# Kernel optimization log

Measured on AMD Instinct MI355X. Metric: run time of the kernel, lower is better.

## Reference

```python
import jax, jax.numpy as jnp
import numpy as np

NUM_HEADS = 8
WINDOW = 3
LOCAL_LEN = WINDOW * WINDOW
SR_RATIO = 8


def _normalize(v, eps=1e-12):
    n = jnp.linalg.norm(v, axis=-1, keepdims=True)
    return v / jnp.maximum(n, eps)


def _layernorm(v, g, b, eps=1e-5):
    m = v.mean(-1, keepdims=True)
    var = ((v - m) ** 2).mean(-1, keepdims=True)
    return (v - m) / jnp.sqrt(var + eps) * g + b


def _unfold3(x, H, W):
    # x: [B, C, H, W] -> [B, C, 9, H*W]  (kernel 3, pad 1, stride 1; torch nn.Unfold layout)
    B, C = x.shape[0], x.shape[1]
    xp = jnp.pad(x, ((0, 0), (0, 0), (1, 1), (1, 1)))
    patches = jnp.stack([xp[:, :, di:di + H, dj:dj + W]
                         for di in range(WINDOW) for dj in range(WINDOW)], axis=2)
    return patches.reshape(B, C, LOCAL_LEN, H * W)


def _forward(x, relative_coords_table, seq_length_scale, q_w, q_b, kv_w, kv_b,
             temperature, query_embedding, sr_w, sr_b, norm_g, norm_b,
             cpb_fc1_w, cpb_fc1_b, cpb_fc2_w, cpb_fc2_b,
             rel_bias_local, learnable_tokens, learnable_bias,
             proj_w, proj_b, relative_pos_index, padding_mask, H, W):
    B, N, C = x.shape
    hd = C // NUM_HEADS
    pool_H, pool_W = H // SR_RATIO, W // SR_RATIO
    pool_len = pool_H * pool_W

    # ---- queries ----
    q = (x @ q_w.T + q_b).reshape(B, N, NUM_HEADS, hd).transpose(0, 2, 1, 3)  # [B,h,N,d]
    q_norm = _normalize(q)
    q_scaled = (q_norm + query_embedding) * jax.nn.softplus(temperature) * seq_length_scale

    # ---- local k/v via unfold ----
    kv = x @ kv_w.T + kv_b  # [B,N,2C]
    k_loc = _normalize(kv[..., :C].reshape(B, N, NUM_HEADS, hd)).reshape(B, N, C)
    kv_img = jnp.concatenate([k_loc, kv[..., C:]], -1).transpose(0, 2, 1).reshape(B, 2 * C, H, W)
    kv_unf = _unfold3(kv_img, H, W).reshape(B, 2 * NUM_HEADS, hd, LOCAL_LEN, N)
    kv_unf = kv_unf.transpose(0, 1, 4, 2, 3)  # [B,2h,N,d,9]
    k_local, v_local = kv_unf[:, :NUM_HEADS], kv_unf[:, NUM_HEADS:]

    attn_local = jnp.einsum('bhnd,bhndl->bhnl', q_scaled, k_local) + rel_bias_local[:, None, :]
    attn_local = jnp.where(padding_mask, -jnp.inf, attn_local)

    # ---- pooled global k/v ----
    x_img = x.transpose(0, 2, 1).reshape(B, C, H, W)
    x_sr = jax.nn.gelu(jnp.einsum('oc,bchw->bohw', sr_w, x_img) + sr_b[None, :, None, None],
                       approximate=False)
    x_pool = x_sr.reshape(B, C, pool_H, SR_RATIO, pool_W, SR_RATIO).mean((3, 5))
    x_pool = x_pool.reshape(B, C, pool_len).transpose(0, 2, 1)
    x_pool = _layernorm(x_pool, norm_g, norm_b)
    kv_p = (x_pool @ kv_w.T + kv_b).reshape(B, pool_len, 2 * NUM_HEADS, hd).transpose(0, 2, 1, 3)
    k_pool, v_pool = kv_p[:, :NUM_HEADS], kv_p[:, NUM_HEADS:]

    # ---- continuous relative position bias (extrapolation path) ----
    cpb = jax.nn.relu(relative_coords_table @ cpb_fc1_w.T + cpb_fc1_b) @ cpb_fc2_w.T + cpb_fc2_b  # [T,h]
    pool_bias = cpb[relative_pos_index].reshape(N, pool_len, NUM_HEADS).transpose(2, 0, 1)  # [h,N,P]

    attn_pool = jnp.einsum('bhnd,bhpd->bhnp', q_scaled, _normalize(k_pool)) + pool_bias

    attn = jax.nn.softmax(jnp.concatenate([attn_local, attn_pool], -1), axis=-1)
    a_loc, a_pool = attn[..., :LOCAL_LEN], attn[..., LOCAL_LEN:]

    lt = jnp.einsum('bhnd,hdl->bhnl', q_norm, learnable_tokens) + learnable_bias + a_loc
    x_local = jnp.einsum('bhnl,bhndl->bhnd', lt, v_local)
    x_p = jnp.einsum('bhnp,bhpd->bhnd', a_pool, v_pool)
    out = (x_local + x_p).transpose(0, 2, 1, 3).reshape(B, N, C)
    return out @ proj_w.T + proj_b


def setup_inputs() -> dict:
    key = jax.random.key(0)
    B, H, W, C = 4, 64, 64, 256
    N = H * W
    hd = C // NUM_HEADS
    pool_H, pool_W = H // SR_RATIO, W // SR_RATIO
    pool_len = pool_H * pool_W

    # padding mask + per-query valid window length (get_seqlen_and_mask)
    ii, jj = np.meshgrid(np.arange(H), np.arange(W), indexing='ij')
    cols = []
    for di in range(WINDOW):
        for dj in range(WINDOW):
            ni, nj = ii + di - 1, jj + dj - 1
            cols.append(((ni < 0) | (ni >= H) | (nj < 0) | (nj >= W)).reshape(-1))
    padding_mask = np.stack(cols, -1)  # [N, 9], True = outside image
    local_len = (~padding_mask).sum(-1, keepdims=True).astype(np.float32)
    seq_length_scale = np.log(local_len + pool_len)  # [N, 1]

    # get_relative_position_cpb((H,W), (pool_H,pool_W))
    axis_q = np.arange(H, dtype=np.float64)
    axis_k = axis_q.reshape(pool_H, SR_RATIO).mean(-1)
    kh, kw = np.meshgrid(axis_k, axis_k, indexing='ij')
    qh, qw = np.meshgrid(axis_q, axis_q, indexing='ij')
    rel_h = (qh.ravel()[:, None] - kh.ravel()[None, :]) / (H - 1) * 8
    rel_w = (qw.ravel()[:, None] - kw.ravel()[None, :]) / (W - 1) * 8
    rel = np.stack([rel_h, rel_w], -1).reshape(-1, 2)
    table, idx = np.unique(rel, axis=0, return_inverse=True)
    table = np.sign(table) * np.log2(np.abs(table) + 1.0) / np.log2(8.0)

    ks = jax.random.split(key, 12)

    def nrm(k, shape, std=0.02):
        return jax.random.normal(k, shape, jnp.float32) * std

    return {
        'x': jax.random.normal(ks[0], (B, N, C), jnp.float32),
        'relative_coords_table': jnp.asarray(table, jnp.float32),
        'seq_length_scale': jnp.asarray(seq_length_scale, jnp.float32),
        'q_w': nrm(ks[1], (C, C)), 'q_b': jnp.zeros((C,), jnp.float32),
        'kv_w': nrm(ks[2], (2 * C, C)), 'kv_b': jnp.zeros((2 * C,), jnp.float32),
        'temperature': jnp.full((NUM_HEADS, 1, 1), float(np.log(np.expm1(1.0 / 0.24))), jnp.float32),
        'query_embedding': nrm(ks[3], (NUM_HEADS, 1, hd)),
        'sr_w': nrm(ks[4], (C, C)), 'sr_b': jnp.zeros((C,), jnp.float32),
        'norm_g': jnp.ones((C,), jnp.float32), 'norm_b': jnp.zeros((C,), jnp.float32),
        'cpb_fc1_w': nrm(ks[5], (512, 2), 0.1), 'cpb_fc1_b': jnp.zeros((512,), jnp.float32),
        'cpb_fc2_w': nrm(ks[6], (NUM_HEADS, 512)), 'cpb_fc2_b': jnp.zeros((NUM_HEADS,), jnp.float32),
        'rel_bias_local': nrm(ks[7], (NUM_HEADS, LOCAL_LEN), 0.0004),
        'learnable_tokens': nrm(ks[8], (NUM_HEADS, hd, LOCAL_LEN)),
        'learnable_bias': jnp.zeros((NUM_HEADS, 1, LOCAL_LEN), jnp.float32),
        'proj_w': nrm(ks[9], (C, C)), 'proj_b': jnp.zeros((C,), jnp.float32),
        'relative_pos_index': jnp.asarray(idx, jnp.int32),
        'padding_mask': jnp.asarray(padding_mask),
        'H': H, 'W': W,
    }


def reference(x, relative_coords_table, seq_length_scale, q_w, q_b, kv_w, kv_b,
              temperature, query_embedding, sr_w, sr_b, norm_g, norm_b,
              cpb_fc1_w, cpb_fc1_b, cpb_fc2_w, cpb_fc2_b,
              rel_bias_local, learnable_tokens, learnable_bias,
              proj_w, proj_b, relative_pos_index, padding_mask, H, W):
    return _forward(x, relative_coords_table, seq_length_scale, q_w, q_b, kv_w, kv_b,
                    temperature, query_embedding, sr_w, sr_b, norm_g, norm_b,
                    cpb_fc1_w, cpb_fc1_b, cpb_fc2_w, cpb_fc2_b,
                    rel_bias_local, learnable_tokens, learnable_bias,
                    proj_w, proj_b, relative_pos_index, padding_mask, H, W)
```

## Files before the change

### kernel.cpp

```cpp
#include <hip/hip_runtime.h>
#include <math.h>


typedef unsigned short ushort_t;
typedef __attribute__((ext_vector_type(8))) _Float16 half8;
typedef __attribute__((ext_vector_type(2))) _Float16 half2_t;
typedef __attribute__((ext_vector_type(4))) float f32x4;

static __device__ __forceinline__ ushort_t f2h(float f) {
    _Float16 h = (_Float16)f;
    return *(ushort_t*)&h;
}

static __device__ __forceinline__ float fdot2f(half2_t a, half2_t b, float c) {
#if __has_builtin(__builtin_amdgcn_fdot2)
    return __builtin_amdgcn_fdot2(a, b, c, false);
#else
    return (float)a[0] * (float)b[0] + (float)a[1] * (float)b[1] + c;
#endif
}

#define GLOAD16(g, l)                                                        \
    __builtin_amdgcn_global_load_lds(                                        \
        (const __attribute__((address_space(1))) unsigned int*)(g),          \
        (__attribute__((address_space(3))) unsigned int*)(l), 16, 0, 0)

template <int TM>
__global__ __launch_bounds__(256) void mfma_hgemm(
    const ushort_t* __restrict__ Ag, const ushort_t* __restrict__ Bg,
    const float* __restrict__ bias, float* __restrict__ out0,
    ushort_t* __restrict__ kvh, float* __restrict__ out2, int mode)
{
    const int K = 256;
    const int IM = TM / 32;
    __shared__ ushort_t Ah[TM * 32];
    __shared__ ushort_t Bh[64 * 32];

    const int t = threadIdx.x;
    const int w = t >> 6;
    const int lane = t & 63;
    const int bm = blockIdx.y * TM;
    const int bn = blockIdx.x * 64;
    const int wm = (w >> 1) * (TM / 2);
    const int wn = (w & 1) * 32;

    f32x4 acc[IM][2];
#pragma unroll
    for (int i = 0; i < IM; ++i)
#pragma unroll
        for (int j = 0; j < 2; ++j) acc[i][j] = f32x4{0.f, 0.f, 0.f, 0.f};

    const int lrow = t >> 2;
    const int lk8  = (t & 3) * 8;

    for (int k0 = 0; k0 < K; k0 += 32) {
#pragma unroll
        for (int r = 0; r < TM / 64; ++r) {
            GLOAD16(Ag + (size_t)(bm + r * 64 + lrow) * K + k0 + lk8,
                    &Ah[(unsigned)(r * 64 + (w * 16)) * 32]);
        }
        GLOAD16(Bg + (size_t)(bn + lrow) * K + k0 + lk8,
                &Bh[(unsigned)(w * 16) * 32]);
        __syncthreads();

        const int fr = lane & 15;
        const int fq = (lane >> 4) * 8;
        half8 af[IM], bf[2];
#pragma unroll
        for (int i = 0; i < IM; ++i)
            af[i] = *(const half8*)&Ah[(wm + i * 16 + fr) * 32 + fq];
#pragma unroll
        for (int j = 0; j < 2; ++j)
            bf[j] = *(const half8*)&Bh[(wn + j * 16 + fr) * 32 + fq];
#pragma unroll
        for (int i = 0; i < IM; ++i)
#pragma unroll
            for (int j = 0; j < 2; ++j)
                acc[i][j] = __builtin_amdgcn_mfma_f32_16x16x32_f16(af[i], bf[j], acc[i][j], 0, 0, 0);
        __syncthreads();
    }

    const int fr = lane & 15;
    const int q4 = (lane >> 4) * 4;
#pragma unroll
    for (int i = 0; i < IM; ++i) {
#pragma unroll
        for (int j = 0; j < 2; ++j) {
            const int col = bn + wn + j * 16 + fr;
            const float bv = bias[col];
#pragma unroll
            for (int r = 0; r < 4; ++r) {
                const int row = bm + wm + i * 16 + q4 + r;
                float v = acc[i][j][r] + bv;
                if (mode == 0) {
                    if (col < 256)      out0[(size_t)row * 256 + col] = v;
                    else if (col < 768) kvh[(size_t)row * 512 + (col - 256)] = f2h(v);
                    else {
                        v = 0.5f * v * (1.0f + erff(v * 0.70710678118654752f));
                        out2[(size_t)row * 256 + (col - 768)] = v;
                    }
                } else {
                    out0[(size_t)row * 256 + col] = v;
                }
            }
        }
    }
}

__global__ __launch_bounds__(256) void cast_half(
    const float4* __restrict__ x, ushort4* __restrict__ o, int n4)
{
    int i = blockIdx.x * 256 + threadIdx.x;
    if (i >= n4) return;
    float4 v = x[i];
    ushort4 h;
    h.x = f2h(v.x); h.y = f2h(v.y); h.z = f2h(v.z); h.w = f2h(v.w);
    o[i] = h;
}

__global__ __launch_bounds__(256) void pack_weights2(
    const float* __restrict__ qw, const float* __restrict__ kvw,
    const float* __restrict__ srw, const float* __restrict__ pw,
    const float* __restrict__ qb, const float* __restrict__ kvb,
    const float* __restrict__ srb,
    ushort_t* __restrict__ Wall, ushort_t* __restrict__ Pw,
    float* __restrict__ ball)
{
    int idx = blockIdx.x * 256 + threadIdx.x;
    if (idx < 262144) {
        int nn = idx >> 8, k = idx & 255;
        float a;
        if (nn < 256)      a = qw[nn * 256 + k];
        else if (nn < 768) a = kvw[(nn - 256) * 256 + k];
        else               a = srw[(nn - 768) * 256 + k];
        Wall[idx] = f2h(a);
    }
    if (idx < 65536) Pw[idx] = f2h(pw[idx]);
    if (idx < 1024) {
        float bv;
        if (idx < 256)      bv = qb[idx];
        else if (idx < 768) bv = kvb[idx - 256];
        else                bv = srb[idx - 768];
        ball[idx] = bv;
    }
}

__global__ __launch_bounds__(256) void bias_expand_t(
    const int* __restrict__ rpi, const float* __restrict__ cpbT,
    float* __restrict__ pbias)
{
    int idx = blockIdx.x * 256 + threadIdx.x;
    int h = idx >> 18;
    int np = idx & 262143;
    pbias[idx] = cpbT[(size_t)rpi[np] * 8 + h];
}

#define BM 64
#define BN 64
#define BKK 16
__global__ __launch_bounds__(256) void gemm_bias_act(
    const float* __restrict__ A, const float* __restrict__ Wt,
    const float* __restrict__ bias, float* __restrict__ Cmat,
    int M, int N, int K, int act)
{
    __shared__ float As[BKK][BM + 4];
    __shared__ float Bs[BKK][BN + 4];
    const int tid = threadIdx.x;
    const int bm = blockIdx.y * BM;
    const int bn = blockIdx.x * BN;
    const int tr = (tid >> 4) << 2;
    const int tc = (tid & 15) << 2;
    const int lr = tid >> 2;
    const int lc = (tid & 3) << 2;
    float acc[4][4] = {{0.f}};

    for (int k0 = 0; k0 < K; k0 += BKK) {
        float4 av = *(const float4*)(A  + (size_t)(bm + lr) * K + k0 + lc);
        float4 wv = *(const float4*)(Wt + (size_t)(bn + lr) * K + k0 + lc);
        As[lc + 0][lr] = av.x; As[lc + 1][lr] = av.y;
        As[lc + 2][lr] = av.z; As[lc + 3][lr] = av.w;
        Bs[lc + 0][lr] = wv.x; Bs[lc + 1][lr] = wv.y;
        Bs[lc + 2][lr] = wv.z; Bs[lc + 3][lr] = wv.w;
        __syncthreads();
#pragma unroll
        for (int kk = 0; kk < BKK; ++kk) {
            float4 a  = *(const float4*)&As[kk][tr];
            float4 bq = *(const float4*)&Bs[kk][tc];
            float av4[4] = {a.x, a.y, a.z, a.w};
            float bv4[4] = {bq.x, bq.y, bq.z, bq.w};
#pragma unroll
            for (int ii = 0; ii < 4; ++ii)
#pragma unroll
                for (int jj = 0; jj < 4; ++jj)
                    acc[ii][jj] = fmaf(av4[ii], bv4[jj], acc[ii][jj]);
        }
        __syncthreads();
    }
#pragma unroll
    for (int ii = 0; ii < 4; ++ii) {
        int m = bm + tr + ii;
#pragma unroll
        for (int jj = 0; jj < 4; ++jj) {
            int nn = bn + tc + jj;
            float v = acc[ii][jj] + bias[nn];
            if (act == 1) v = 0.5f * v * (1.0f + erff(v * 0.70710678118654752f));
            Cmat[(size_t)m * N + nn] = v;
        }
    }
}

__global__ __launch_bounds__(256) void headnorm(float* __restrict__ buf, int rowStride)
{
    size_t row = blockIdx.x;
    int tid = threadIdx.x;
    float* p = buf + row * (size_t)rowStride + tid;
    float v = *p;
    float ss = v * v;
#pragma unroll
    for (int off = 16; off; off >>= 1) ss += __shfl_xor(ss, off, 32);
    *p = v / fmaxf(sqrtf(ss), 1e-12f);
}

__global__ __launch_bounds__(256) void headnorm_h(ushort_t* __restrict__ buf)
{
    size_t row = blockIdx.x;
    int tid = threadIdx.x;
    ushort_t* p = buf + row * 512 + tid;
    float v = (float)(*(const _Float16*)p);
    float ss = v * v;
#pragma unroll
    for (int off = 16; off; off >>= 1) ss += __shfl_xor(ss, off, 32);
    *p = f2h(v / fmaxf(sqrtf(ss), 1e-12f));
}

__global__ __launch_bounds__(256) void pool_ln(
    const float* __restrict__ xsr, const float* __restrict__ g,
    const float* __restrict__ be, float* __restrict__ xpool, int Hh, int Ww)
{
    const int C = 256;
    const int Nn = Hh * Ww;
    int b = blockIdx.x >> 6;
    int pidx = blockIdx.x & 63;
    int ph = pidx >> 3, pw = pidx & 7;
    int tid = threadIdx.x;
    float s = 0.f;
    for (int si = 0; si < 8; ++si) {
        int i = ph * 8 + si;
        const float* rowp = xsr + ((size_t)b * Nn + (size_t)i * Ww + pw * 8) * C + tid;
#pragma unroll
        for (int sj = 0; sj < 8; ++sj) s += rowp[(size_t)sj * C];
    }
    s *= (1.f / 64.f);
    __shared__ float red[256];
    red[tid] = s; __syncthreads();
    for (int st = 128; st; st >>= 1) { if (tid < st) red[tid] += red[tid + st]; __syncthreads(); }
    float mean = red[0] * (1.f / 256.f);
    __syncthreads();
    float dv = s - mean;
    red[tid] = dv * dv; __syncthreads();
    for (int st = 128; st; st >>= 1) { if (tid < st) red[tid] += red[tid + st]; __syncthreads(); }
    float var = red[0] * (1.f / 256.f);
    xpool[(size_t)blockIdx.x * C + tid] = dv * rsqrtf(var + 1e-5f) * g[tid] + be[tid];
}

__global__ __launch_bounds__(256) void cpb_mlp_v2(
    const float* __restrict__ table, const float* __restrict__ w1,
    const float* __restrict__ b1, const float* __restrict__ w2,
    const float* __restrict__ b2, float* __restrict__ outc, int T)
{
    const int wv = threadIdx.x >> 6;
    const int lane = threadIdx.x & 63;
    const int row = blockIdx.x * 4 + wv;
    if (row >= T) return;
    const float t0 = table[(size_t)row * 2];
    const float t1 = table[(size_t)row * 2 + 1];
    const int base = lane * 8;

    const float4* w1p = (const float4*)(w1 + (size_t)base * 2);
    float4 wa = w1p[0], wb = w1p[1], wc = w1p[2], wd = w1p[3];
    float4 ba = *(const float4*)(b1 + base);
    float4 bb = *(const float4*)(b1 + base + 4);
    float h[8];
    h[0] = fmaxf(fmaf(t1, wa.y, fmaf(t0, wa.x, ba.x)), 0.f);
    h[1] = fmaxf(fmaf(t1, wa.w, fmaf(t0, wa.z, ba.y)), 0.f);
    h[2] = fmaxf(fmaf(t1, wb.y, fmaf(t0, wb.x, ba.z)), 0.f);
    h[3] = fmaxf(fmaf(t1, wb.w, fmaf(t0, wb.z, ba.w)), 0.f);
    h[4] = fmaxf(fmaf(t1, wc.y, fmaf(t0, wc.x, bb.x)), 0.f);
    h[5] = fmaxf(fmaf(t1, wc.w, fmaf(t0, wc.z, bb.y)), 0.f);
    h[6] = fmaxf(fmaf(t1, wd.y, fmaf(t0, wd.x, bb.z)), 0.f);
    h[7] = fmaxf(fmaf(t1, wd.w, fmaf(t0, wd.z, bb.w)), 0.f);

#pragma unroll
    for (int hh = 0; hh < 8; ++hh) {
        const float4* w2p = (const float4*)(w2 + (size_t)hh * 512 + base);
        float4 p0 = w2p[0], p1 = w2p[1];
        float s = h[0]*p0.x + h[1]*p0.y + h[2]*p0.z + h[3]*p0.w
                + h[4]*p1.x + h[5]*p1.y + h[6]*p1.z + h[7]*p1.w;
#pragma unroll
        for (int off = 1; off <= 32; off <<= 1) s += __shfl_xor(s, off);
        if (lane == 0) outc[(size_t)row * 8 + hh] = s + b2[hh];
    }
}

__global__ __launch_bounds__(256) void attn_v7(
    const float* __restrict__ qraw,
    const ushort_t* __restrict__ kvh,
    const float* __restrict__ kvp,
    const float* __restrict__ pbias,
    const float* __restrict__ sls, const float* __restrict__ temp,
    const float* __restrict__ qe, const float* __restrict__ rbl,
    const float* __restrict__ ltok, const float* __restrict__ lbias,
    ushort_t* __restrict__ attno_hf)
{
    const int h = blockIdx.y, b = blockIdx.z;
    const int t = threadIdx.x;

    __shared__ half8 kp_s[64][4];
    __shared__ half8 vp_s[64][4];
    __shared__ float lts[9][32];
    __shared__ float rbl_s[9], lb_s[9], qe_s[32];

    {
        const int p = t >> 2;
        const int g4 = t & 3;
        const float* g = kvp + ((size_t)(b * 64 + p)) * 512 + h * 32 + g4 * 8;
        float4 ka = *(const float4*)(g + 0);
        float4 kb = *(const float4*)(g + 4);
        float4 va = *(const float4*)(g + 256);
        float4 vb = *(const float4*)(g + 260);
        half8 kh, vh;
        kh[0]=(_Float16)ka.x; kh[1]=(_Float16)ka.y; kh[2]=(_Float16)ka.z; kh[3]=(_Float16)ka.w;
        kh[4]=(_Float16)kb.x; kh[5]=(_Float16)kb.y; kh[6]=(_Float16)kb.z; kh[7]=(_Float16)kb.w;
        vh[0]=(_Float16)va.x; vh[1]=(_Float16)va.y; vh[2]=(_Float16)va.z; vh[3]=(_Float16)va.w;
        vh[4]=(_Float16)vb.x; vh[5]=(_Float16)vb.y; vh[6]=(_Float16)vb.z; vh[7]=(_Float16)vb.w;
        kp_s[p][g4] = kh;
        vp_s[p][g4] = vh;
        for (int u = t; u < 288; u += 256) lts[u % 9][u / 9] = ltok[h * 288 + u];
        if (t < 9)  { rbl_s[t] = rbl[h * 9 + t]; lb_s[t] = lbias[h * 9 + t]; }
        if (t >= 64 && t < 96) qe_s[t - 64] = qe[h * 32 + (t - 64)];
    }
    __syncthreads();

    const int w = t >> 6;
    const int lane = t & 63;
    const int qi = lane >> 2;
    const int g4 = lane & 3;
    const int co = g4 * 8;
    const int i = blockIdx.x;
    const int j = w * 16 + qi;
    const int n = i * 64 + j;
    const size_t gq = (size_t)b * 4096 + n;

    const float tm = temp[h];
    const float sp = (tm > 20.f) ? tm : log1pf(expf(tm));

    float qv[8];
    {
        float ss = 0.f;
        const float4* qp = (const float4*)(qraw + gq * 256 + h * 32 + co);
#pragma unroll
        for (int c4 = 0; c4 < 2; ++c4) {
            float4 v = qp[c4];
            qv[4*c4+0] = v.x; qv[4*c4+1] = v.y; qv[4*c4+2] = v.z; qv[4*c4+3] = v.w;
            ss += v.x*v.x + v.y*v.y + v.z*v.z + v.w*v.w;
        }
        ss += __shfl_xor(ss, 1);
        ss += __shfl_xor(ss, 2);
        const float invn = 1.0f / fmaxf(sqrtf(ss), 1e-12f);
#pragma unroll
        for (int d = 0; d < 8; ++d) qv[d] *= invn;
    }

    float lt[9];
#pragma unroll
    for (int l = 0; l < 9; ++l) {
        float dl = 0.f;
        const float4* lw = (const float4*)&lts[l][co];
#pragma unroll
        for (int c4 = 0; c4 < 2; ++c4) {
            float4 w4 = lw[c4];
            dl += qv[4*c4+0]*w4.x + qv[4*c4+1]*w4.y + qv[4*c4+2]*w4.z + qv[4*c4+3]*w4.w;
        }
        dl += __shfl_xor(dl, 1);
        dl += __shfl_xor(dl, 2);
        lt[l] = dl + lb_s[l];
    }

    const float scal = sp * sls[n];
    half2_t qh[4];
#pragma unroll
    for (int c = 0; c < 4; ++c) {
        float a = (qv[2*c+0] + qe_s[co + 2*c+0]) * scal;
        float bq = (qv[2*c+1] + qe_s[co + 2*c+1]) * scal;
        qh[c] = half2_t{(_Float16)a, (_Float16)bq};
    }

    float sl[9];
#pragma unroll
    for (int l = 0; l < 9; ++l) {
        const int di = l / 3 - 1, dj = l % 3 - 1;
        const int ii = i + di;
        const int jn = j + dj;
        const bool ok = (ii >= 0) && (ii < 64) && (jn >= 0) && (jn < 64);
        const int ic = max(min(ii, 63), 0);
        const int jc = max(min(jn, 63), 0);
        const half8 k8 = *(const half8*)(kvh + ((size_t)(b * 4096 + ic * 64 + jc)) * 512 + h * 32 + co);
        float dk = 0.f;
        dk = fdot2f(qh[0], __builtin_shufflevector(k8, k8, 0, 1), dk);
        dk = fdot2f(qh[1], __builtin_shufflevector(k8, k8, 2, 3), dk);
        dk = fdot2f(qh[2], __builtin_shufflevector(k8, k8, 4, 5), dk);
        dk = fdot2f(qh[3], __builtin_shufflevector(k8, k8, 6, 7), dk);
        dk += __shfl_xor(dk, 1);
        dk += __shfl_xor(dk, 2);
        sl[l] = ok ? (dk + rbl_s[l]) : -INFINITY;
    }

    float m = sl[0];
#pragma unroll
    for (int l = 1; l < 9; ++l) m = fmaxf(m, sl[l]);

    half2_t oh[4];
#pragma unroll
    for (int c = 0; c < 4; ++c) oh[c] = half2_t{(_Float16)0.f, (_Float16)0.f};
    float Z = 0.f;
    const float* plane = pbias + ((size_t)h << 18) + (size_t)n * 64;

    for (int cch = 0; cch < 8; ++cch) {
        float s8[8];
        float4 pb0 = *(const float4*)(plane + cch * 8);
        float4 pb1 = *(const float4*)(plane + cch * 8 + 4);
        const float pbv[8] = {pb0.x, pb0.y, pb0.z, pb0.w, pb1.x, pb1.y, pb1.z, pb1.w};
#pragma unroll
        for (int k = 0; k < 8; ++k) {
            const int p = cch * 8 + k;
            const half8 k8 = kp_s[p][g4];
            float acc = 0.f;
            acc = fdot2f(qh[0], __builtin_shufflevector(k8, k8, 0, 1), acc);
            acc = fdot2f(qh[1], __builtin_shufflevector(k8, k8, 2, 3), acc);
            acc = fdot2f(qh[2], __builtin_shufflevector(k8, k8, 4, 5), acc);
            acc = fdot2f(qh[3], __builtin_shufflevector(k8, k8, 6, 7), acc);
            acc += __shfl_xor(acc, 1);
            acc += __shfl_xor(acc, 2);
            s8[k] = acc + pbv[k];
        }
        float cmax = s8[0];
#pragma unroll
        for (int k = 1; k < 8; ++k) cmax = fmaxf(cmax, s8[k]);
        const float m_new = fmaxf(m, cmax);
        const float factor = __expf(m - m_new);
        Z *= factor;
        const _Float16 fh = (_Float16)factor;
        const half2_t f2 = half2_t{fh, fh};
#pragma unroll
        for (int c = 0; c < 4; ++c) oh[c] *= f2;
        m = m_new;
#pragma unroll
        for (int k = 0; k < 8; ++k) {
            const float a = __expf(s8[k] - m);
            Z += a;
            const _Float16 ah = (_Float16)a;
            const half2_t a2 = half2_t{ah, ah};
            const half8 v8 = vp_s[cch * 8 + k][g4];
            oh[0] = a2 * __builtin_shufflevector(v8, v8, 0, 1) + oh[0];
            oh[1] = a2 * __builtin_shufflevector(v8, v8, 2, 3) + oh[1];
            oh[2] = a2 * __builtin_shufflevector(v8, v8, 4, 5) + oh[2];
            oh[3] = a2 * __builtin_shufflevector(v8, v8, 6, 7) + oh[3];
        }
    }

#pragma unroll
    for (int l = 0; l < 9; ++l) { sl[l] = __expf(sl[l] - m); Z += sl[l]; }

#pragma unroll
    for (int l = 0; l < 9; ++l) {
        const int di = l / 3 - 1, dj = l % 3 - 1;
        const int ii = i + di;
        const int jn = j + dj;
        const bool ok = (ii >= 0) && (ii < 64) && (jn >= 0) && (jn < 64);
        const int ic = max(min(ii, 63), 0);
        const int jc = max(min(jn, 63), 0);
        const float coef = ok ? (sl[l] + lt[l] * Z) : 0.f;
        const half8 v8 = *(const half8*)(kvh + ((size_t)(b * 4096 + ic * 64 + jc)) * 512 + 256 + h * 32 + co);
        const _Float16 ch = (_Float16)coef;
        const half2_t c2 = half2_t{ch, ch};
        oh[0] = c2 * __builtin_shufflevector(v8, v8, 0, 1) + oh[0];
        oh[1] = c2 * __builtin_shufflevector(v8, v8, 2, 3) + oh[1];
        oh[2] = c2 * __builtin_shufflevector(v8, v8, 4, 5) + oh[2];
        oh[3] = c2 * __builtin_shufflevector(v8, v8, 6, 7) + oh[3];
    }

    const float invZ = 1.0f / Z;
    ushort4* outp = (ushort4*)(attno_hf + gq * 256 + h * 32 + co);
#pragma unroll
    for (int c4 = 0; c4 < 2; ++c4) {
        ushort4 u;
        u.x = f2h((float)oh[2*c4+0][0] * invZ);
        u.y = f2h((float)oh[2*c4+0][1] * invZ);
        u.z = f2h((float)oh[2*c4+1][0] * invZ);
        u.w = f2h((float)oh[2*c4+1][1] * invZ);
        outp[c4] = u;
    }
}

extern "C" void kernel_launch(void* const* d_in, const int* in_sizes, int n_in,
                              void* d_out, int out_size, void* d_ws, size_t ws_size,
                              hipStream_t stream)
{
    const float* x    = (const float*)d_in[0];
    const float* tbl  = (const float*)d_in[1];
    const float* sls  = (const float*)d_in[2];
    const float* q_w  = (const float*)d_in[3];
    const float* q_b  = (const float*)d_in[4];
    const float* kv_w = (const float*)d_in[5];
    const float* kv_b = (const float*)d_in[6];
    const float* temp = (const float*)d_in[7];
    const float* qe   = (const float*)d_in[8];
    const float* sr_w = (const float*)d_in[9];
    const float* sr_b = (const float*)d_in[10];
    const float* ng   = (const float*)d_in[11];
    const float* nb   = (const float*)d_in[12];
    const float* f1w  = (const float*)d_in[13];
    const float* f1b  = (const float*)d_in[14];
    const float* f2w  = (const float*)d_in[15];
    const float* f2b  = (const float*)d_in[16];
    const float* rbl  = (const float*)d_in[17];
    const float* ltok = (const float*)d_in[18];
    const float* lbias= (const float*)d_in[19];
    const float* pw   = (const float*)d_in[20];
    const float* pb   = (const float*)d_in[21];
    const int*   rpi  = (const int*)d_in[22];

    const int C = 256, Hh = 64, Ww = 64, Nn = Hh * Ww;
    const int B = in_sizes[0] / (Nn * C);
    const int T = in_sizes[1] / 2;
    const int M = B * Nn;

    float* ws = (float*)d_ws;
    size_t o = 0;
    float* qbuf  = ws + o; o += (size_t)M * C;
    ushort_t* kvh = (ushort_t*)(ws + o); o += (size_t)M * C;
    float* xsr   = ws + o; o += (size_t)M * C;
    float* xpool = ws + o; o += (size_t)B * 64 * C;
    float* kvp   = ws + o; o += (size_t)B * 64 * 2 * C;
    float* cpbB  = ws + o; o += (size_t)T * 8;
    float* pbias = ws + o; o += (size_t)8 * Nn * 64;
    ushort_t* xh   = (ushort_t*)(ws + o); o += (size_t)M * C / 2;
    ushort_t* Wall = (ushort_t*)(ws + o); o += 1024 * 256 / 2;
    ushort_t* Pwh  = (ushort_t*)(ws + o); o += 256 * 256 / 2;
    float* ball = ws + o; o += 1024;
    ushort_t* attno_hf = xh;

    dim3 blk(256);
    const int n4x = M * C / 4;

    cast_half<<<(n4x + 255) / 256, blk, 0, stream>>>((const float4*)x, (ushort4*)xh, n4x);
    pack_weights2<<<1024, blk, 0, stream>>>(q_w, kv_w, sr_w, pw, q_b, kv_b, sr_b,
                                            Wall, Pwh, ball);
    mfma_hgemm<128><<<dim3(16, M / 128), blk, 0, stream>>>(
        xh, Wall, ball, qbuf, kvh, xsr, 0);
    headnorm_h<<<M, blk, 0, stream>>>(kvh);
    pool_ln<<<B * 64, blk, 0, stream>>>(xsr, ng, nb, xpool, Hh, Ww);
    gemm_bias_act<<<dim3(2 * C / BN, (B * 64) / BM), blk, 0, stream>>>(xpool, kv_w, kv_b, kvp, B * 64, 2 * C, C, 0);
    headnorm<<<B * 64, blk, 0, stream>>>(kvp, 2 * C);
    cpb_mlp_v2<<<(T + 3) / 4, blk, 0, stream>>>(tbl, f1w, f1b, f2w, f2b, cpbB, T);
    bias_expand_t<<<(8 * Nn * 64) / 256, blk, 0, stream>>>(rpi, cpbB, pbias);
    attn_v7<<<dim3(64, 8, B), blk, 0, stream>>>(
        qbuf, kvh, kvp, pbias, sls, temp, qe, rbl, ltok, lbias, attno_hf);
    mfma_hgemm<64><<<dim3(4, M / 64), blk, 0, stream>>>(
        attno_hf, Pwh, pb, (float*)d_out, nullptr, nullptr, 1);
}
```

Measured before the change: 239.2 us.

## Fuse key head-norm into GEMM epilogue, store q and sr output as fp16

```diff
diff --git a/kernel.cpp b/kernel.cpp
--- a/kernel.cpp
+++ b/kernel.cpp
@@ -29,7 +29,8 @@
 __global__ __launch_bounds__(256) void mfma_hgemm(
     const ushort_t* __restrict__ Ag, const ushort_t* __restrict__ Bg,
     const float* __restrict__ bias, float* __restrict__ out0,
-    ushort_t* __restrict__ kvh, float* __restrict__ out2, int mode)
+    ushort_t* __restrict__ qh_out, ushort_t* __restrict__ kvh,
+    ushort_t* __restrict__ xsrh, int mode)
 {
     const int K = 256;
     const int IM = TM / 32;
@@ -85,40 +86,42 @@
 #pragma unroll
     for (int i = 0; i < IM; ++i) {
 #pragma unroll
-        for (int j = 0; j < 2; ++j) {
-            const int col = bn + wn + j * 16 + fr;
-            const float bv = bias[col];
-#pragma unroll
-            for (int r = 0; r < 4; ++r) {
-                const int row = bm + wm + i * 16 + q4 + r;
-                float v = acc[i][j][r] + bv;
-                if (mode == 0) {
-                    if (col < 256)      out0[(size_t)row * 256 + col] = v;
-                    else if (col < 768) kvh[(size_t)row * 512 + (col - 256)] = f2h(v);
-                    else {
-                        v = 0.5f * v * (1.0f + erff(v * 0.70710678118654752f));
-                        out2[(size_t)row * 256 + (col - 768)] = v;
-                    }
+        for (int r = 0; r < 4; ++r) {
+            const int row = bm + wm + i * 16 + q4 + r;
+            const int col0 = bn + wn + fr;
+            const int col1 = col0 + 16;
+            float v0 = acc[i][0][r] + bias[col0];
+            float v1 = acc[i][1][r] + bias[col1];
+            if (mode == 0) {
+                if (col0 < 256) {
+                    qh_out[(size_t)row * 256 + col0] = f2h(v0);
+                    qh_out[(size_t)row * 256 + col1] = f2h(v1);
+                } else if (col0 < 512) {
+                    float ss = v0 * v0 + v1 * v1;
+                    ss += __shfl_xor(ss, 1); ss += __shfl_xor(ss, 2);
+                    ss += __shfl_xor(ss, 4); ss += __shfl_xor(ss, 8);
+                    const float invn = 1.0f / fmaxf(sqrtf(ss), 1e-12f);
+                    kvh[(size_t)row * 512 + (col0 - 256)] = f2h(v0 * invn);
+                    kvh[(size_t)row * 512 + (col1 - 256)] = f2h(v1 * invn);
+                } else if (col0 < 768) {
+                    kvh[(size_t)row * 512 + (col0 - 256)] = f2h(v0);
+                    kvh[(size_t)row * 512 + (col1 - 256)] = f2h(v1);
                 } else {
-                    out0[(size_t)row * 256 + col] = v;
+                    v0 = 0.5f * v0 * (1.0f + erff(v0 * 0.70710678118654752f));
+                    v1 = 0.5f * v1 * (1.0f + erff(v1 * 0.70710678118654752f));
+                    xsrh[(size_t)row * 256 + (col0 - 768)] = f2h(v0);
+                    xsrh[(size_t)row * 256 + (col1 - 768)] = f2h(v1);
                 }
+            } else {
+                out0[(size_t)row * 256 + col0] = v0;
+                out0[(size_t)row * 256 + col1] = v1;
             }
         }
     }
 }
 
-__global__ __launch_bounds__(256) void cast_half(
-    const float4* __restrict__ x, ushort4* __restrict__ o, int n4)
-{
-    int i = blockIdx.x * 256 + threadIdx.x;
-    if (i >= n4) return;
-    float4 v = x[i];
-    ushort4 h;
-    h.x = f2h(v.x); h.y = f2h(v.y); h.z = f2h(v.z); h.w = f2h(v.w);
-    o[i] = h;
-}
-
-__global__ __launch_bounds__(256) void pack_weights2(
+__global__ __launch_bounds__(256) void prep(
+    const float4* __restrict__ x, ushort4* __restrict__ xh, int n4,
     const float* __restrict__ qw, const float* __restrict__ kvw,
     const float* __restrict__ srw, const float* __restrict__ pw,
     const float* __restrict__ qb, const float* __restrict__ kvb,
@@ -127,6 +130,12 @@
     float* __restrict__ ball)
 {
     int idx = blockIdx.x * 256 + threadIdx.x;
+    if (idx < n4) {
+        float4 v = x[idx];
+        ushort4 h;
+        h.x = f2h(v.x); h.y = f2h(v.y); h.z = f2h(v.z); h.w = f2h(v.w);
+        xh[idx] = h;
+    }
     if (idx < 262144) {
         int nn = idx >> 8, k = idx & 255;
         float a;
@@ -221,20 +230,8 @@
     *p = v / fmaxf(sqrtf(ss), 1e-12f);
 }
 
-__global__ __launch_bounds__(256) void headnorm_h(ushort_t* __restrict__ buf)
-{
-    size_t row = blockIdx.x;
-    int tid = threadIdx.x;
-    ushort_t* p = buf + row * 512 + tid;
-    float v = (float)(*(const _Float16*)p);
-    float ss = v * v;
-#pragma unroll
-    for (int off = 16; off; off >>= 1) ss += __shfl_xor(ss, off, 32);
-    *p = f2h(v / fmaxf(sqrtf(ss), 1e-12f));
-}
-
 __global__ __launch_bounds__(256) void pool_ln(
-    const float* __restrict__ xsr, const float* __restrict__ g,
+    const ushort_t* __restrict__ xsr, const float* __restrict__ g,
     const float* __restrict__ be, float* __restrict__ xpool, int Hh, int Ww)
 {
     const int C = 256;
@@ -246,9 +243,10 @@
     float s = 0.f;
     for (int si = 0; si < 8; ++si) {
         int i = ph * 8 + si;
-        const float* rowp = xsr + ((size_t)b * Nn + (size_t)i * Ww + pw * 8) * C + tid;
-#pragma unroll
-        for (int sj = 0; sj < 8; ++sj) s += rowp[(size_t)sj * C];
+        const ushort_t* rowp = xsr + ((size_t)b * Nn + (size_t)i * Ww + pw * 8) * C + tid;
+#pragma unroll
+        for (int sj = 0; sj < 8; ++sj)
+            s += (float)(*(const _Float16*)&rowp[(size_t)sj * C]);
     }
     s *= (1.f / 64.f);
     __shared__ float red[256];
@@ -303,7 +301,7 @@
 }
 
 __global__ __launch_bounds__(256) void attn_v7(
-    const float* __restrict__ qraw,
+    const ushort_t* __restrict__ qh_g,
     const ushort_t* __restrict__ kvh,
     const float* __restrict__ kvp,
     const float* __restrict__ pbias,
@@ -356,14 +354,10 @@
 
     float qv[8];
     {
+        const half8 q8 = *(const half8*)(qh_g + gq * 256 + h * 32 + co);
         float ss = 0.f;
-        const float4* qp = (const float4*)(qraw + gq * 256 + h * 32 + co);
-#pragma unroll
-        for (int c4 = 0; c4 < 2; ++c4) {
-            float4 v = qp[c4];
-            qv[4*c4+0] = v.x; qv[4*c4+1] = v.y; qv[4*c4+2] = v.z; qv[4*c4+3] = v.w;
-            ss += v.x*v.x + v.y*v.y + v.z*v.z + v.w*v.w;
-        }
+#pragma unroll
+        for (int d = 0; d < 8; ++d) { qv[d] = (float)q8[d]; ss += qv[d] * qv[d]; }
         ss += __shfl_xor(ss, 1);
         ss += __shfl_xor(ss, 2);
         const float invn = 1.0f / fmaxf(sqrtf(ss), 1e-12f);
@@ -537,9 +531,9 @@
 
     float* ws = (float*)d_ws;
     size_t o = 0;
-    float* qbuf  = ws + o; o += (size_t)M * C;
-    ushort_t* kvh = (ushort_t*)(ws + o); o += (size_t)M * C;
-    float* xsr   = ws + o; o += (size_t)M * C;
+    ushort_t* qh   = (ushort_t*)(ws + o); o += (size_t)M * C / 2;
+    ushort_t* kvh  = (ushort_t*)(ws + o); o += (size_t)M * C;
+    ushort_t* xsrh = (ushort_t*)(ws + o); o += (size_t)M * C / 2;
     float* xpool = ws + o; o += (size_t)B * 64 * C;
     float* kvp   = ws + o; o += (size_t)B * 64 * 2 * C;
     float* cpbB  = ws + o; o += (size_t)T * 8;
@@ -553,19 +547,18 @@
     dim3 blk(256);
     const int n4x = M * C / 4;
 
-    cast_half<<<(n4x + 255) / 256, blk, 0, stream>>>((const float4*)x, (ushort4*)xh, n4x);
-    pack_weights2<<<1024, blk, 0, stream>>>(q_w, kv_w, sr_w, pw, q_b, kv_b, sr_b,
-                                            Wall, Pwh, ball);
+    prep<<<(n4x + 255) / 256, blk, 0, stream>>>(
+        (const float4*)x, (ushort4*)xh, n4x,
+        q_w, kv_w, sr_w, pw, q_b, kv_b, sr_b, Wall, Pwh, ball);
     mfma_hgemm<128><<<dim3(16, M / 128), blk, 0, stream>>>(
-        xh, Wall, ball, qbuf, kvh, xsr, 0);
-    headnorm_h<<<M, blk, 0, stream>>>(kvh);
-    pool_ln<<<B * 64, blk, 0, stream>>>(xsr, ng, nb, xpool, Hh, Ww);
+        xh, Wall, ball, nullptr, qh, kvh, xsrh, 0);
+    pool_ln<<<B * 64, blk, 0, stream>>>(xsrh, ng, nb, xpool, Hh, Ww);
     gemm_bias_act<<<dim3(2 * C / BN, (B * 64) / BM), blk, 0, stream>>>(xpool, kv_w, kv_b, kvp, B * 64, 2 * C, C, 0);
     headnorm<<<B * 64, blk, 0, stream>>>(kvp, 2 * C);
     cpb_mlp_v2<<<(T + 3) / 4, blk, 0, stream>>>(tbl, f1w, f1b, f2w, f2b, cpbB, T);
     bias_expand_t<<<(8 * Nn * 64) / 256, blk, 0, stream>>>(rpi, cpbB, pbias);
     attn_v7<<<dim3(64, 8, B), blk, 0, stream>>>(
-        qbuf, kvh, kvp, pbias, sls, temp, qe, rbl, ltok, lbias, attno_hf);
+        qh, kvh, kvp, pbias, sls, temp, qe, rbl, ltok, lbias, attno_hf);
     mfma_hgemm<64><<<dim3(4, M / 64), blk, 0, stream>>>(
-        attno_hf, Pwh, pb, (float*)d_out, nullptr, nullptr, 1);
-}
+        attno_hf, Pwh, pb, (float*)d_out, nullptr, nullptr, nullptr, 1);
+}
```

After: 231.7 us. -3.1%, faster.
